# Performance work log

Hardware: AMD Instinct MI355X
Metric: run time of the kernel (lower is better)

Reference implementation:

```python
import jax, jax.numpy as jnp
import numpy as np

D_MODEL = 1024
NUM_HEADS = 16
HEAD_DIM = D_MODEL // NUM_HEADS
THETA = 10000.0
B, S = 2, 2048


def _apply_rope(t, cos, sin):
    # t: [B, H, S, hd]; cos/sin: [S, hd//2]
    te = t[..., 0::2]
    to = t[..., 1::2]
    re = te * cos - to * sin
    ro = te * sin + to * cos
    out = jnp.stack([re, ro], axis=-1)  # [B,H,S,hd//2,2]
    return out.reshape(t.shape)


def setup_inputs() -> dict:
    key = jax.random.key(0)
    kx, kq, kk, kv, ko = jax.random.split(key, 5)
    std = 2.0 / (2 * D_MODEL) ** 0.5
    def w(k):
        return jnp.clip(std * jax.random.normal(k, (D_MODEL, D_MODEL), jnp.float32), -3.0 * std, 3.0 * std)
    return {
        "x": jax.random.normal(kx, (B, S, D_MODEL), jnp.float32),
        "Wq": w(kq),
        "Wk": w(kk),
        "Wv": w(kv),
        "Wo": w(ko),
    }


def reference(x, Wq, Wk, Wv, Wo):
    Bv, Sv, _ = x.shape
    def proj(W):
        return jnp.einsum('bsd,ed->bse', x, W).reshape(Bv, Sv, NUM_HEADS, HEAD_DIM).transpose(0, 2, 1, 3)
    q, k, v = proj(Wq), proj(Wk), proj(Wv)

    pos = jnp.arange(Sv, dtype=jnp.float32)
    inv_freq = THETA ** (-jnp.arange(0, HEAD_DIM, 2, dtype=jnp.float32) / HEAD_DIM)
    ang = pos[:, None] * inv_freq[None, :]  # [S, hd//2]
    cos, sin = jnp.cos(ang), jnp.sin(ang)
    q = _apply_rope(q, cos, sin)
    k = _apply_rope(k, cos, sin)

    scale = 1.0 / jnp.sqrt(jnp.float32(HEAD_DIM))
    scores = jnp.einsum('bhqd,bhkd->bhqk', q.astype(jnp.float32), k.astype(jnp.float32)) * scale
    causal = jnp.tril(jnp.ones((Sv, Sv), dtype=bool))
    scores = jnp.where(causal[None, None], scores, -jnp.inf)
    attn = jax.nn.softmax(scores, axis=-1)
    out = jnp.einsum('bhqk,bhkd->bhqd', attn, v.astype(jnp.float32))
    out = out.transpose(0, 2, 1, 3).reshape(Bv, Sv, D_MODEL)
    return jnp.einsum('bsd,ed->bse', out, Wo)
```

## Files before the change

kernel.cpp:

```cpp
#include <hip/hip_runtime.h>
#include <hip/hip_bf16.h>
#include <stdint.h>

typedef __bf16 bf16x8 __attribute__((ext_vector_type(8)));
typedef float  f32x4  __attribute__((ext_vector_type(4)));

__device__ __forceinline__ float bf2f(unsigned short u) {
    union { float f; uint32_t i; } v; v.i = ((uint32_t)u) << 16; return v.f;
}
__device__ __forceinline__ unsigned short f2bf(float f) {
    union { float f; uint32_t i; } v; v.f = f;
    uint32_t r = v.i + 0x7FFF + ((v.i >> 16) & 1);
    return (unsigned short)(r >> 16);
}
__device__ __forceinline__ unsigned short f2bf_rz(float f) {
    union { float f; uint32_t i; } v; v.f = f;
    return (unsigned short)(v.i >> 16);
}

#define GLD_LDS(gptr, lptr) \
    __builtin_amdgcn_global_load_lds( \
        (const __attribute__((address_space(1))) void*)(gptr), \
        (__attribute__((address_space(3))) void*)(lptr), 16, 0, 0)

__global__ __launch_bounds__(256) void convert_inputs(
    const void* __restrict__ x,  const void* __restrict__ wq,
    const void* __restrict__ wk, const void* __restrict__ wv,
    const void* __restrict__ wo, unsigned short* __restrict__ dst,
    unsigned short* __restrict__ wob_dst, int* __restrict__ flag)
{
    __shared__ int cnt[256];
    const int tid = threadIdx.x;
    uint32_t u = ((const uint32_t*)x)[tid];
    int e = (u >> 7) & 0xFF;
    cnt[tid] = (e >= 100 && e <= 140) ? 1 : 0;
    __syncthreads();
    for (int s = 128; s > 0; s >>= 1) {
        if (tid < s) cnt[tid] += cnt[tid + s];
        __syncthreads();
    }
    const int isf32 = (cnt[0] >= 128) ? 0 : 1;
    if (blockIdx.x == 0 && tid == 0) flag[0] = isf32 ? 0 : 1;

    int c = blockIdx.x * 256 + tid;
    const void* src; size_t off; unsigned short* out;
    if (c < 524288)      { src = x;  off = (size_t)c * 8;            out = dst + (size_t)c * 8; }
    else if (c < 655360) { src = wq; off = (size_t)(c - 524288) * 8; out = dst + (size_t)c * 8; }
    else if (c < 786432) { src = wk; off = (size_t)(c - 655360) * 8; out = dst + (size_t)c * 8; }
    else if (c < 917504) { src = wv; off = (size_t)(c - 786432) * 8; out = dst + (size_t)c * 8; }
    else                 { src = wo; off = (size_t)(c - 917504) * 8; out = wob_dst + off; }
    unsigned short t[8];
    if (isf32) {
        const float* s = (const float*)src + off;
        float4 f0 = *(const float4*)s;
        float4 f1 = *(const float4*)(s + 4);
        t[0] = f2bf(f0.x); t[1] = f2bf(f0.y); t[2] = f2bf(f0.z); t[3] = f2bf(f0.w);
        t[4] = f2bf(f1.x); t[5] = f2bf(f1.y); t[6] = f2bf(f1.z); t[7] = f2bf(f1.w);
    } else {
        *(uint4*)t = *(const uint4*)((const unsigned short*)src + off);
    }
    *(uint4*)out = *(const uint4*)t;
}

__global__ __launch_bounds__(512, 2) void gemm_qkv_8ph(
    const unsigned short* __restrict__ A,
    const unsigned short* __restrict__ B0,
    const unsigned short* __restrict__ B1,
    const unsigned short* __restrict__ B2,
    unsigned short* __restrict__ O0,
    unsigned short* __restrict__ O1,
    unsigned short* __restrict__ O2)
{
    __shared__ __align__(16) unsigned short Asl[2][16384];
    __shared__ __align__(16) unsigned short Bsl[2][16384];

    const int tid  = threadIdx.x;
    const int lane = tid & 63;
    const int wid  = tid >> 6;
    const int wm   = wid >> 2;
    const int wn   = wid & 3;
    const int lr   = lane & 15;
    const int quad = lane >> 4;

    const int bid   = blockIdx.x;
    const int xcd   = bid & 7;
    const int s_    = bid >> 3;
    const int m_idx = xcd + 8 * (s_ / 12);
    const int n_idx = s_ % 12;

    const int m0  = m_idx * 256;
    const int n0g = n_idx * 256;
    const int sel = n0g >> 10;
    const unsigned short* Bp = (sel == 0) ? B0 : ((sel == 1) ? B1 : B2);
    unsigned short* Optr     = (sel == 0) ? O0 : ((sel == 1) ? O1 : O2);
    const int n0  = n0g & 1023;

    const int sw0 = ((0 + quad) ^ (lr & 7)) * 8;
    const int sw1 = ((4 + quad) ^ (lr & 7)) * 8;

    f32x4 acc[2][4][2][2] = {};
    bf16x8 aF[4][2];
    bf16x8 bF[2][2];

#define STAGEA(T, H) do { \
    const int tA_ = (T); \
    _Pragma("unroll") \
    for (int p_ = 0; p_ < 2; ++p_) { \
        int c_   = p_ * 512 + tid; \
        int row_ = c_ >> 3; \
        int sc_  = ((c_ & 7) ^ (row_ & 7)) * 8; \
        GLD_LDS(&A[(size_t)(m0 + (H) * 128 + row_) * 1024 + tA_ * 64 + sc_], \
                &Asl[tA_ & 1][(H) * 8192 + c_ * 8]); \
    } } while (0)

#define STAGEB(T, H) do { \
    const int tB_ = (T); \
    _Pragma("unroll") \
    for (int p_ = 0; p_ < 2; ++p_) { \
        int c_   = p_ * 512 + tid; \
        int row_ = c_ >> 3; \
        int sc_  = ((c_ & 7) ^ (row_ & 7)) * 8; \
        GLD_LDS(&Bp[(size_t)(n0 + (H) * 128 + row_) * 1024 + tB_ * 64 + sc_], \
                &Bsl[tB_ & 1][(H) * 8192 + c_ * 8]); \
    } } while (0)

#define LOADA(BUF, QM) do { \
    _Pragma("unroll") \
    for (int fm_ = 0; fm_ < 4; ++fm_) { \
        const int row_ = (QM) * 128 + wm * 64 + fm_ * 16 + lr; \
        aF[fm_][0] = *(const bf16x8*)&Asl[BUF][row_ * 64 + sw0]; \
        aF[fm_][1] = *(const bf16x8*)&Asl[BUF][row_ * 64 + sw1]; \
    } } while (0)

#define LOADB(BUF, QN) do { \
    _Pragma("unroll") \
    for (int fn_ = 0; fn_ < 2; ++fn_) { \
        const int row_ = (QN) * 128 + wn * 32 + fn_ * 16 + lr; \
        bF[fn_][0] = *(const bf16x8*)&Bsl[BUF][row_ * 64 + sw0]; \
        bF[fn_][1] = *(const bf16x8*)&Bsl[BUF][row_ * 64 + sw1]; \
    } } while (0)

#define MFMA16(QM, QN) do { \
    __builtin_amdgcn_s_setprio(1); \
    _Pragma("unroll") \
    for (int fm_ = 0; fm_ < 4; ++fm_) { \
        _Pragma("unroll") \
        for (int fn_ = 0; fn_ < 2; ++fn_) { \
            acc[QM][fm_][QN][fn_] = __builtin_amdgcn_mfma_f32_16x16x32_bf16( \
                aF[fm_][0], bF[fn_][0], acc[QM][fm_][QN][fn_], 0, 0, 0); \
            acc[QM][fm_][QN][fn_] = __builtin_amdgcn_mfma_f32_16x16x32_bf16( \
                aF[fm_][1], bF[fn_][1], acc[QM][fm_][QN][fn_], 0, 0, 0); \
        } \
    } \
    __builtin_amdgcn_s_setprio(0); \
    } while (0)

#define BARRIER() __builtin_amdgcn_s_barrier()
#define LGKM0()   asm volatile("s_waitcnt lgkmcnt(0)" ::: "memory")

    STAGEB(0, 0);
    STAGEA(0, 1);
    STAGEA(0, 0);
    STAGEB(0, 1);
    STAGEB(1, 0);
    STAGEA(1, 1);
    asm volatile("s_waitcnt vmcnt(4)" ::: "memory");
    BARRIER();

    const int NT = 16;
#pragma unroll 2
    for (int t = 0; t < NT; ++t) {
        const int buf = t & 1;

        LOADA(buf, 0);
        LOADB(buf, 0);
        if (t + 1 < NT) STAGEA(t + 1, 0);
        BARRIER();
        LGKM0();
        MFMA16(0, 0);
        BARRIER();

        LOADA(buf, 1);
        if (t + 1 < NT) STAGEB(t + 1, 1);
        BARRIER();
        LGKM0();
        MFMA16(1, 0);
        BARRIER();

        LOADB(buf, 1);
        if (t + 2 < NT) STAGEB(t + 2, 0);
        BARRIER();
        LGKM0();
        MFMA16(1, 1);
        BARRIER();

        LOADA(buf, 0);
        if (t + 2 < NT) STAGEA(t + 2, 1);
        BARRIER();
        LGKM0();
        MFMA16(0, 1);
        if (t + 2 < NT) asm volatile("s_waitcnt vmcnt(4)" ::: "memory");
        else            asm volatile("s_waitcnt vmcnt(0)" ::: "memory");
        BARRIER();
    }

#pragma unroll
    for (int qm = 0; qm < 2; ++qm) {
#pragma unroll
        for (int fm = 0; fm < 4; ++fm) {
            const int mb = m0 + qm * 128 + wm * 64 + fm * 16 + quad * 4;
#pragma unroll
            for (int qn = 0; qn < 2; ++qn) {
#pragma unroll
                for (int fn = 0; fn < 2; ++fn) {
                    const int nl = n0 + qn * 128 + wn * 32 + fn * 16 + lr;
                    const int h = nl >> 6, d = nl & 63;
#pragma unroll
                    for (int r = 0; r < 4; ++r) {
                        const int m = mb + r;
                        const int b = m >> 11, s = m & 2047;
                        Optr[((size_t)(b * 16 + h) * 2048 + s) * 64 + d] =
                            f2bf(acc[qm][fm][qn][fn][r]);
                    }
                }
            }
        }
    }
#undef STAGEA
#undef STAGEB
#undef LOADA
#undef LOADB
#undef MFMA16
#undef BARRIER
#undef LGKM0
}

__global__ __launch_bounds__(256) void gemm_out(
    const unsigned short* __restrict__ P0,
    const unsigned short* __restrict__ P1,
    const float* __restrict__ Lsum,
    const unsigned short* __restrict__ B0,
    void* __restrict__ O,
    const int* __restrict__ flag)
{
    const int K = 1024;
    __shared__ __align__(16) unsigned short As[64 * 64];
    __shared__ __align__(16) unsigned short Bs[128 * 64];

    const int isf32 = (flag[0] == 0) ? 1 : 0;

    const int tid  = threadIdx.x;
    const int lane = tid & 63;
    const int wid  = tid >> 6;
    const int wm   = wid >> 1;
    const int wn   = wid & 1;
    const int lr   = lane & 15;
    const int quad = lane >> 4;
    const int q8   = quad * 8;

    const int bid   = blockIdx.x;
    const int xcd   = bid & 7;
    const int s_    = bid >> 3;
    const int m_idx = xcd + 8 * (s_ >> 3);
    const int n_idx = s_ & 7;

    const int m0 = m_idx * 64;
    const int n0 = n_idx * 128;

    f32x4 acc[2][4] = {};

    for (int kk = 0; kk < K; kk += 64) {
        __syncthreads();
        const int h = kk >> 6;
        for (int p = 0; p < 2; ++p) {
            int c   = p * 256 + tid;
            int row = c >> 3;
            int d0  = (c & 7) * 8;
            int m   = m0 + row;
            int b   = m >> 11, s = m & 2047;
            int li  = (b * 16 + h) * 2048 + s;
            float inv = 1.0f / (Lsum[li] + Lsum[65536 + li]);
            size_t addr = ((size_t)li) * 64 + d0;
            unsigned short a[8], bb[8], o[8];
            *(uint4*)a  = *(const uint4*)&P0[addr];
            *(uint4*)bb = *(const uint4*)&P1[addr];
            for (int j = 0; j < 8; ++j)
                o[j] = f2bf((bf2f(a[j]) + bf2f(bb[j])) * inv);
            *(uint4*)&As[c * 8] = *(const uint4*)o;
        }
        for (int p = 0; p < 4; ++p) {
            int c   = p * 256 + tid;
            int row = c >> 3;
            int c8  = (c & 7) * 8;
            GLD_LDS(&B0[(size_t)(n0 + row) * K + kk + c8], &Bs[c * 8]);
        }
        __syncthreads();

        for (int ks = 0; ks < 64; ks += 32) {
            bf16x8 af[2], bf[4];
            for (int t = 0; t < 2; ++t)
                af[t] = *(const bf16x8*)&As[(wm * 32 + t * 16 + lr) * 64 + ks + q8];
            for (int t = 0; t < 4; ++t)
                bf[t] = *(const bf16x8*)&Bs[(wn * 64 + t * 16 + lr) * 64 + ks + q8];
            for (int mt = 0; mt < 2; ++mt)
                for (int nt = 0; nt < 4; ++nt)
                    acc[mt][nt] = __builtin_amdgcn_mfma_f32_16x16x32_bf16(
                        af[mt], bf[nt], acc[mt][nt], 0, 0, 0);
        }
    }

    for (int mt = 0; mt < 2; ++mt) {
        for (int nt = 0; nt < 4; ++nt) {
            for (int r = 0; r < 4; ++r) {
                int m  = m0 + wm * 32 + mt * 16 + quad * 4 + r;
                int nl = n0 + wn * 64 + nt * 16 + lr;
                float val = acc[mt][nt][r];
                if (isf32) ((float*)O)[(size_t)m * 1024 + nl] = val;
                else ((unsigned short*)O)[(size_t)m * 1024 + nl] = f2bf(val);
            }
        }
    }
}

__global__ __launch_bounds__(256) void rope_transpose(
    unsigned short* __restrict__ Q, unsigned short* __restrict__ Kp,
    const unsigned short* __restrict__ V, unsigned short* __restrict__ Vt)
{
    __shared__ unsigned short T[64 * 65];
    const int tid = threadIdx.x;

    if (blockIdx.x < 4096) {
        const int CH = 32 * 2048 * 8;
        int idx = blockIdx.x * 256 + tid;
        bool isK = idx >= CH;
        int j = isK ? (idx - CH) : idx;
        unsigned short* p = isK ? Kp : Q;

        int c8   = j & 7;
        int srow = j >> 3;
        int s    = srow & 2047;
        int off  = srow * 64 + c8 * 8;

        uint4 raw = *(const uint4*)&p[off];
        unsigned short t[8];
        *(uint4*)t = raw;
        float sf = (float)s;
        float qs = isK ? 1.0f : 0.125f;
        for (int jj = 0; jj < 4; ++jj) {
            int i = c8 * 4 + jj;
            float inv = __expf(-0.2878231366f * (float)i);
            float ang = sf * inv;
            float sn = __sinf(ang);
            float cs = __cosf(ang);
            float e = bf2f(t[2 * jj]);
            float o = bf2f(t[2 * jj + 1]);
            t[2 * jj]     = f2bf((e * cs - o * sn) * qs);
            t[2 * jj + 1] = f2bf((e * sn + o * cs) * qs);
        }
        *(uint4*)&p[off] = *(const uint4*)t;
    } else {
        int bidx = blockIdx.x - 4096;
        const int s0 = (bidx & 31) * 64;
        const int bh = bidx >> 5;

        const unsigned short* src = V + ((size_t)bh * 2048 + s0) * 64;
        for (int p = 0; p < 2; ++p) {
            int c = p * 256 + tid;
            int s  = c >> 3;
            int d8 = (c & 7) * 8;
            uint4 raw = *(const uint4*)&src[s * 64 + d8];
            unsigned short t[8];
            *(uint4*)t = raw;
            for (int j = 0; j < 8; ++j) T[s * 65 + d8 + j] = t[j];
        }
        __syncthreads();
        unsigned short* dst = Vt + (size_t)bh * 64 * 2048 + s0;
        for (int p = 0; p < 2; ++p) {
            int c = p * 256 + tid;
            int d  = c >> 3;
            int s8 = (c & 7) * 8;
            unsigned short t[8];
            for (int j = 0; j < 8; ++j) t[j] = T[(s8 + j) * 65 + d];
            *(uint4*)&dst[(size_t)d * 2048 + s8] = *(const uint4*)t;
        }
    }
}

__global__ __launch_bounds__(256) void attn_kernel(
    const unsigned short* __restrict__ Q,
    const unsigned short* __restrict__ Kp,
    const unsigned short* __restrict__ Vt,
    unsigned short* __restrict__ P0,
    unsigned short* __restrict__ P1,
    float* __restrict__ Lsum)
{
    __shared__ __align__(16) unsigned short Ks[2][4096];
    __shared__ __align__(16) unsigned short Vs[2][4096];
    __shared__ __align__(16) unsigned short Ps[4096];

    const int tid  = threadIdx.x;
    const int lane = tid & 63;
    const int w    = tid >> 6;
    const int lr   = lane & 15;
    const int quad = lane >> 4;
    const int q8   = quad * 8;
    const int wps  = w * 1024;

    const int bh    = blockIdx.x;
    const int y     = blockIdx.y;
    const int split = y >> 4;
    const int yq    = y & 15;
    const int qb    = (yq < 8) ? yq : (23 - yq);
    const int q0    = qb * 128;
    const int kb0   = split ? (qb + 1) : 0;
    const int kb1   = split ? (2 * qb + 1) : qb;

    unsigned short* Pout = split ? P1 : P0;

    const unsigned short* KbBase = Kp + (size_t)bh * 2048 * 64;
    const unsigned short* VbBase = Vt + (size_t)bh * 131072;

    auto stage = [&](int kb, int buf) {
        const unsigned short* Kb = KbBase + kb * 64 * 64;
        const unsigned short* Vb = VbBase + kb * 64;
        for (int p = 0; p < 2; ++p) {
            int c    = p * 256 + tid;
            int f    = c >> 6, l = c & 63;
            int nt   = f >> 1, ks = f & 1;
            int lr_s = l & 15, qd = l >> 4;
            GLD_LDS(&Kb[(nt * 16 + lr_s) * 64 + ks * 32 + qd * 8], &Ks[buf][c * 8]);
            GLD_LDS(&Vb[(size_t)(nt * 16 + lr_s) * 2048 + ks * 32 + qd * 8], &Vs[buf][c * 8]);
        }
    };

    bf16x8 qa[2][2];
    for (int mt = 0; mt < 2; ++mt) {
        const unsigned short* Qw = Q + ((size_t)bh * 2048 + q0 + mt * 64 + w * 16 + lr) * 64;
        qa[mt][0] = *(const bf16x8*)&Qw[q8];
        qa[mt][1] = *(const bf16x8*)&Qw[32 + q8];
    }

    stage(kb0, 0);

    f32x4 oacc[2][4] = {};
    float lpart[2][4] = {};
    const int l8 = lane * 8;
    const int lr7 = lr & 7;
    const int lrh = lr >> 3;

    for (int kb = kb0; kb <= kb1; ++kb) {
        const int cur = (kb - kb0) & 1;
        __syncthreads();
        if (kb < kb1) stage(kb + 1, cur ^ 1);

        f32x4 sacc[2][4] = {};
        for (int nt = 0; nt < 4; ++nt) {
            bf16x8 kf0 = *(const bf16x8*)&Ks[cur][(nt * 2 + 0) * 512 + l8];
            bf16x8 kf1 = *(const bf16x8*)&Ks[cur][(nt * 2 + 1) * 512 + l8];
            for (int mt = 0; mt < 2; ++mt) {
                sacc[mt][nt] = __builtin_amdgcn_mfma_f32_16x16x32_bf16(qa[mt][0], kf0, sacc[mt][nt], 0, 0, 0);
                sacc[mt][nt] = __builtin_amdgcn_mfma_f32_16x16x32_bf16(qa[mt][1], kf1, sacc[mt][nt], 0, 0, 0);
            }
        }

        if (kb >= 2 * qb) {
            for (int mt = 0; mt < 2; ++mt) {
                int rowb = q0 + mt * 64 + w * 16 + quad * 4;
                for (int nt = 0; nt < 4; ++nt) {
                    int col = kb * 64 + nt * 16 + lr;
                    for (int r = 0; r < 4; ++r)
                        if (col > rowb + r) sacc[mt][nt][r] = -3.0e38f;
                }
            }
        }

        for (int mt = 0; mt < 2; ++mt) {
            for (int r = 0; r < 4; ++r) {
                for (int nt = 0; nt < 4; ++nt) {
                    float pv = __expf(sacc[mt][nt][r] - 16.0f);
                    lpart[mt][r] += pv;
                    int ks = nt >> 1;
                    int qr = (nt * 2 + lrh) & 3;
                    Ps[wps + ks * 512 + (qr * 16 + quad * 4 + r) * 8 + lr7] = f2bf_rz(pv);
                }
            }
            for (int ks = 0; ks < 2; ++ks) {
                bf16x8 pa = *(const bf16x8*)&Ps[wps + ks * 512 + l8];
                for (int nt = 0; nt < 4; ++nt) {
                    bf16x8 vf = *(const bf16x8*)&Vs[cur][(nt * 2 + ks) * 512 + l8];
                    oacc[mt][nt] = __builtin_amdgcn_mfma_f32_16x16x32_bf16(pa, vf, oacc[mt][nt], 0, 0, 0);
                }
            }
        }
    }

    for (int mt = 0; mt < 2; ++mt) {
        for (int r = 0; r < 4; ++r) {
            float l = lpart[mt][r];
            for (int off = 1; off < 16; off <<= 1)
                l += __shfl_xor(l, off, 64);
            int s = q0 + mt * 64 + w * 16 + quad * 4 + r;
            for (int nt = 0; nt < 4; ++nt)
                Pout[((size_t)bh * 2048 + s) * 64 + nt * 16 + lr] = f2bf_rz(oacc[mt][nt][r]);
            if (lr == 0) Lsum[split * 65536 + bh * 2048 + s] = l;
        }
    }
}

extern "C" void kernel_launch(void* const* d_in, const int* in_sizes, int n_in,
                              void* d_out, int out_size, void* d_ws, size_t ws_size,
                              hipStream_t stream)
{
    const void* x  = d_in[0];
    const void* Wq = d_in[1];
    const void* Wk = d_in[2];
    const void* Wv = d_in[3];
    const void* Wo = d_in[4];

    int* flag = (int*)d_ws;
    unsigned short* base = (unsigned short*)d_ws + 8;
    const size_t M1 = 1048576;
    unsigned short* xb  = base;
    unsigned short* wqb = base + 4 * M1;
    unsigned short* wkb = base + 5 * M1;
    unsigned short* wvb = base + 6 * M1;
    unsigned short* q   = base + 8 * M1;
    unsigned short* k   = base + 12 * M1;
    unsigned short* v   = base + 16 * M1;
    unsigned short* wob = base + 20 * M1;
    float*          Ls  = (float*)(base + 21 * M1);
    unsigned short* vt  = xb;
    unsigned short* P0  = v;
    unsigned short* P1  = wqb;

    convert_inputs<<<dim3(4096), 256, 0, stream>>>(x, Wq, Wk, Wv, Wo, base, wob, flag);
    gemm_qkv_8ph<<<dim3(192), 512, 0, stream>>>(xb, wqb, wkb, wvb, q, k, v);
    rope_transpose<<<dim3(5120), 256, 0, stream>>>(q, k, v, vt);
    attn_kernel<<<dim3(32, 32), 256, 0, stream>>>(q, k, vt, P0, P1, Ls);
    gemm_out<<<dim3(512), 256, 0, stream>>>(P0, P1, Ls, wob, d_out, flag);
}
```

Before: 212.7 us.

## Split causal attention KV range four ways with longest-first block ordering

Adds a four-way split of each query block's key range in the attention kernel. Blocks are launched on a flat 2048-block grid ordered from the longest query rows to the shortest, so the causal triangle's work is balanced across more, smaller blocks. Each split writes its own partial output and row sum, and the output projection now sums four partials instead of two before normalising. The new path is used only when the workspace is large enough to hold the extra partial buffers; otherwise the old two-split path runs. The cost is extra partial-output traffic plus additional loads and adds in the output GEMM prologue.

```diff
diff --git a/kernel.cpp b/kernel.cpp
--- a/kernel.cpp
+++ b/kernel.cpp
@@ -235,9 +235,12 @@
 #undef LGKM0
 }
 
+template<int NS>
 __global__ __launch_bounds__(256) void gemm_out(
     const unsigned short* __restrict__ P0,
     const unsigned short* __restrict__ P1,
+    const unsigned short* __restrict__ P2,
+    const unsigned short* __restrict__ P3,
     const float* __restrict__ Lsum,
     const unsigned short* __restrict__ B0,
     void* __restrict__ O,
@@ -279,13 +282,23 @@
             int m   = m0 + row;
             int b   = m >> 11, s = m & 2047;
             int li  = (b * 16 + h) * 2048 + s;
-            float inv = 1.0f / (Lsum[li] + Lsum[65536 + li]);
+            float lsum = Lsum[li] + Lsum[65536 + li];
+            if (NS == 4) lsum += Lsum[131072 + li] + Lsum[196608 + li];
+            float inv = 1.0f / lsum;
             size_t addr = ((size_t)li) * 64 + d0;
             unsigned short a[8], bb[8], o[8];
             *(uint4*)a  = *(const uint4*)&P0[addr];
             *(uint4*)bb = *(const uint4*)&P1[addr];
-            for (int j = 0; j < 8; ++j)
-                o[j] = f2bf((bf2f(a[j]) + bf2f(bb[j])) * inv);
+            if (NS == 4) {
+                unsigned short c2[8], d2[8];
+                *(uint4*)c2 = *(const uint4*)&P2[addr];
+                *(uint4*)d2 = *(const uint4*)&P3[addr];
+                for (int j = 0; j < 8; ++j)
+                    o[j] = f2bf((bf2f(a[j]) + bf2f(bb[j]) + bf2f(c2[j]) + bf2f(d2[j])) * inv);
+            } else {
+                for (int j = 0; j < 8; ++j)
+                    o[j] = f2bf((bf2f(a[j]) + bf2f(bb[j])) * inv);
+            }
             *(uint4*)&As[c * 8] = *(const uint4*)o;
         }
         for (int p = 0; p < 4; ++p) {
@@ -386,12 +399,15 @@
     }
 }
 
+template<int NSPLIT>
 __global__ __launch_bounds__(256) void attn_kernel(
     const unsigned short* __restrict__ Q,
     const unsigned short* __restrict__ Kp,
     const unsigned short* __restrict__ Vt,
     unsigned short* __restrict__ P0,
     unsigned short* __restrict__ P1,
+    unsigned short* __restrict__ P2,
+    unsigned short* __restrict__ P3,
     float* __restrict__ Lsum)
 {
     __shared__ __align__(16) unsigned short Ks[2][4096];
@@ -406,16 +422,28 @@
     const int q8   = quad * 8;
     const int wps  = w * 1024;
 
-    const int bh    = blockIdx.x;
-    const int y     = blockIdx.y;
-    const int split = y >> 4;
-    const int yq    = y & 15;
-    const int qb    = (yq < 8) ? yq : (23 - yq);
-    const int q0    = qb * 128;
-    const int kb0   = split ? (qb + 1) : 0;
-    const int kb1   = split ? (2 * qb + 1) : qb;
-
-    unsigned short* Pout = split ? P1 : P0;
+    int bh, split, qb, kb0, kb1;
+    if (NSPLIT == 2) {
+        bh = blockIdx.x;
+        const int y  = blockIdx.y;
+        split = y >> 4;
+        const int yq = y & 15;
+        qb  = (yq < 8) ? yq : (23 - yq);
+        kb0 = split ? (qb + 1) : 0;
+        kb1 = split ? (2 * qb + 1) : qb;
+    } else {
+        const int idx = blockIdx.x;
+        qb    = 15 - (idx >> 7);
+        const int r = idx & 127;
+        split = r >> 5;
+        bh    = r & 31;
+        const int L = 2 * qb + 2;
+        kb0 = (L * split) >> 2;
+        kb1 = ((L * (split + 1)) >> 2) - 1;
+    }
+
+    unsigned short* Pout = (split == 0) ? P0 : (split == 1) ? P1
+                         : (split == 2) ? P2 : P3;
 
     const unsigned short* KbBase = Kp + (size_t)bh * 2048 * 64;
     const unsigned short* VbBase = Vt + (size_t)bh * 131072;
@@ -433,6 +461,7 @@
         }
     };
 
+    const int q0 = qb * 128;
     bf16x8 qa[2][2];
     for (int mt = 0; mt < 2; ++mt) {
         const unsigned short* Qw = Q + ((size_t)bh * 2048 + q0 + mt * 64 + w * 16 + lr) * 64;
@@ -532,10 +561,19 @@
     unsigned short* vt  = xb;
     unsigned short* P0  = v;
     unsigned short* P1  = wqb;
+    unsigned short* P2  = base + 22 * M1;
+    unsigned short* P3  = base + 26 * M1;
+
+    const bool big = ws_size >= (size_t)30 * M1 * 2 + 16;
 
     convert_inputs<<<dim3(4096), 256, 0, stream>>>(x, Wq, Wk, Wv, Wo, base, wob, flag);
     gemm_qkv_8ph<<<dim3(192), 512, 0, stream>>>(xb, wqb, wkb, wvb, q, k, v);
     rope_transpose<<<dim3(5120), 256, 0, stream>>>(q, k, v, vt);
-    attn_kernel<<<dim3(32, 32), 256, 0, stream>>>(q, k, vt, P0, P1, Ls);
-    gemm_out<<<dim3(512), 256, 0, stream>>>(P0, P1, Ls, wob, d_out, flag);
-}
+    if (big) {
+        attn_kernel<4><<<dim3(2048), 256, 0, stream>>>(q, k, vt, P0, P1, P2, P3, Ls);
+        gemm_out<4><<<dim3(512), 256, 0, stream>>>(P0, P1, P2, P3, Ls, wob, d_out, flag);
+    } else {
+        attn_kernel<2><<<dim3(32, 32), 256, 0, stream>>>(q, k, vt, P0, P1, P0, P0, Ls);
+        gemm_out<2><<<dim3(512), 256, 0, stream>>>(P0, P1, P0, P0, Ls, wob, d_out, flag);
+    }
+}
```

After: 216.1 us. About the same (+1.6%).
